# Kernel tuning notes

Hardware: AMD Instinct MI355X
Metric: run time of the kernel (lower is better)

Reference implementation:

```python
import jax, jax.numpy as jnp
import numpy as np

NUM_CODEBOOKS = 4
CODEBOOK_SIZE = 4096
CODEBOOK_DIM = 512


def setup_inputs() -> dict:
    key = jax.random.key(0)
    k1, k2 = jax.random.split(key)
    inputs = jax.random.normal(k1, (8, 2048, CODEBOOK_DIM), dtype=jnp.float32)
    # nn.init.uniform_(codebook.weight, -1/codebook_size, 1/codebook_size)
    bound = 1.0 / CODEBOOK_SIZE
    codebook = jax.random.uniform(k2, (CODEBOOK_SIZE, CODEBOOK_DIM),
                                  dtype=jnp.float32, minval=-bound, maxval=bound)
    return {"inputs": inputs, "codebook": codebook}


def reference(inputs, codebook):
    original_shape = inputs.shape
    x = inputs.reshape(-1, CODEBOOK_DIM)  # [N, D]
    cb_sq = jnp.sum(codebook ** 2, axis=1)  # [K]

    def stage(residual, _):
        # distances: ||r||^2 - 2 r.W^T + ||w||^2  -> [N, K]
        distances = (jnp.sum(residual ** 2, axis=1, keepdims=True)
                     - 2.0 * residual @ codebook.T
                     + cb_sq[None, :])
        indices = jnp.argmin(distances, axis=-1)  # [N]
        # one-hot matmul in torch == gather; same math
        quantized = codebook[indices]  # [N, D]
        # straight-through estimator
        q_ste = residual + jax.lax.stop_gradient(quantized - residual)
        new_residual = residual - q_ste
        return new_residual, (q_ste, indices)

    _, (q_stages, idx_stages) = jax.lax.scan(stage, x, None, length=NUM_CODEBOOKS)
    quantized_out = jnp.sum(q_stages, axis=0).reshape(original_shape)
    # all_indices stacked along last dim: [B, T, num_codebooks]
    all_indices = jnp.moveaxis(idx_stages, 0, -1).reshape(*original_shape[:-1], NUM_CODEBOOKS)
    vq_loss = jnp.float32(0.0)  # eval mode: self.training is False
    return quantized_out, all_indices, vq_loss
```

## Files before the change

### kernel.cpp

```cpp
#include <hip/hip_runtime.h>
#include <math.h>


namespace {
constexpr int N_ROWS     = 16384;
constexpr int DIM        = 512;
constexpr int K_CODES    = 4096;
constexpr int NUM_STAGES = 4;

constexpr int KTILES = 32;
constexpr float EPS  = 1e-3f;
constexpr int CAP    = 2;

constexpr int CROWS  = 32;
constexpr int CGRIDY = 8;
constexpr int WSTRC  = 68;
constexpr int RSTR   = 68;

constexpr size_t Q_OFF    = 0;
constexpr size_t IDX_OFF  = (size_t)N_ROWS * DIM;
constexpr size_t LOSS_OFF = IDX_OFF + (size_t)N_ROWS * NUM_STAGES;

constexpr size_t RES_OFF  = 0;
constexpr size_t RH_OFF   = (size_t)N_ROWS * DIM * 4;
constexpr size_t WH_OFF   = RH_OFF + (size_t)N_ROWS * DIM * 2;
constexpr size_t CBSQ_OFF = WH_OFF + (size_t)K_CODES * DIM * 2;
constexpr size_t RSQ_OFF  = CBSQ_OFF + (size_t)K_CODES * 4;
constexpr size_t PART_OFF = RSQ_OFF + (size_t)N_ROWS * 4;
constexpr size_t GBUF_OFF = PART_OFF + (size_t)N_ROWS * KTILES * 4;
constexpr size_t BCNT_OFF = GBUF_OFF + (size_t)N_ROWS * KTILES * CAP * 8;
constexpr size_t BENT_OFF = BCNT_OFF + 128;
constexpr size_t BEST_OFF = BENT_OFF + (size_t)KTILES * N_ROWS * 4;

constexpr unsigned long long EMPTY_E = 0xFFFFFFFFFFFFFFFFull;
constexpr unsigned long long OVFL_E  = 0xFFFFFFFFFFFFFFFEull;
}

typedef short bf16x8 __attribute__((ext_vector_type(8)));
typedef float f32x4  __attribute__((ext_vector_type(4)));

typedef __attribute__((address_space(1))) const unsigned int glob_u32;
typedef __attribute__((address_space(3))) unsigned int lds_u32;

__device__ __forceinline__ unsigned short f2bf(float x) {
    unsigned int u = __float_as_uint(x);
    return (unsigned short)((u + 0x7fffu + ((u >> 16) & 1u)) >> 16);
}

__device__ __forceinline__ float f4c(const float4& v, int q) {
    return q == 0 ? v.x : q == 1 ? v.y : q == 2 ? v.z : v.w;
}

__device__ __forceinline__ float rowsq_tree(const float v8[8], int lane) {
#pragma clang fp contract(off)
    float P[4];
#pragma unroll
    for (int b = 0; b < 4; ++b) {
        float xa = v8[2 * b];
        float xb = v8[2 * b + 1];
        float sa = xa * xa;
        float sb = xb * xb;
        float R  = sa + sb;
        float t  = R + __shfl_down(R, 16, 64);
        float u  = t + __shfl_down(t, 32, 64);
        float a  = u + __shfl_down(u, 8, 64);
        float c  = a + __shfl_down(a, 4, 64);
        float d  = c + __shfl_down(c, 2, 64);
        P[b]     = d + __shfl_down(d, 1, 64);
    }
    float s01 = P[0] + P[1];
    float s23 = P[2] + P[3];
    return s01 + s23;
}

__global__ __launch_bounds__(64)
void cbsq_wh_kernel(const float* __restrict__ cb, float* __restrict__ cb_sq,
                    unsigned short* __restrict__ wh, float* __restrict__ loss) {
    int k = blockIdx.x;
    int lane = threadIdx.x;
    const float* row = cb + (size_t)k * DIM;
    unsigned short* whp = wh + (size_t)k * DIM;
    float v8[8];
#pragma unroll
    for (int i = 0; i < 8; ++i) {
        float v = row[lane + i * 64];
        v8[i] = v;
        whp[lane + i * 64] = f2bf(v);
    }
    float s = rowsq_tree(v8, lane);
    if (lane == 0) cb_sq[k] = s;
    if (k == 0 && lane == 0) *loss = 0.0f;
}

__global__ __launch_bounds__(256)
void init_kernel(const float* __restrict__ input,
                 unsigned short* __restrict__ rh,
                 float* __restrict__ rsq, int* __restrict__ bcnt) {
    const int t = threadIdx.x;
    if (blockIdx.x == 0 && t < KTILES) bcnt[t] = 0;
    const int lane = t & 63;
    const int sub  = t >> 6;
    const int row  = blockIdx.x * 4 + sub;
    const float* x = input + (size_t)row * DIM;
    unsigned short* rhp = rh + (size_t)row * DIM;
    float v8[8];
#pragma unroll
    for (int i = 0; i < 8; ++i) {
        int d = lane + i * 64;
        float v = x[d];
        v8[i] = v;
        rhp[d] = f2bf(v);
    }
    float s = rowsq_tree(v8, lane);
    if (lane == 0) rsq[row] = s;
}

__global__ __launch_bounds__(256, 2)
void passA_kernel(const unsigned short* __restrict__ rh,
                  const unsigned short* __restrict__ wh,
                  const float* __restrict__ cb_sq,
                  const float* __restrict__ rsq,
                  float* __restrict__ part,
                  unsigned long long* __restrict__ gbuf) {
    const int lin = blockIdx.x + KTILES * blockIdx.y;
    const int xcd = lin & 7;
    const int c   = lin >> 3;
    const int jb  = c & 31;
    const int mb  = xcd * 16 + (c >> 5);
    const int mbase = mb * 128;
    const int nbase = jb * 128;

    __shared__ __align__(16) unsigned short At[128 * 64];
    __shared__ __align__(16) unsigned short Bt[128 * 64];
    __shared__ float rowmin[128][2];

    const int t    = threadIdx.x;
    const int lane = t & 63;
    const int wid  = t >> 6;
    const int wr   = wid >> 1;
    const int wc   = wid & 1;

    const int lrow = lane >> 3;
    const int d8g  = (lane & 7) ^ lrow;

    f32x4 acc[4][4];
#pragma unroll
    for (int mi = 0; mi < 4; ++mi)
#pragma unroll
        for (int ni = 0; ni < 4; ++ni) acc[mi][ni] = (f32x4){0.f, 0.f, 0.f, 0.f};

    for (int k0 = 0; k0 < DIM; k0 += 64) {
#pragma unroll
        for (int i = 0; i < 4; ++i) {
            int rbase = wid * 32 + i * 8;
            int grow  = rbase + lrow;
            const unsigned short* ga =
                rh + (size_t)(mbase + grow) * DIM + k0 + d8g * 8;
            __builtin_amdgcn_global_load_lds(
                (glob_u32*)ga, (lds_u32*)&At[rbase * 64], 16, 0, 0);
            const unsigned short* gb =
                wh + (size_t)(nbase + grow) * DIM + k0 + d8g * 8;
            __builtin_amdgcn_global_load_lds(
                (glob_u32*)gb, (lds_u32*)&Bt[rbase * 64], 16, 0, 0);
        }
        __syncthreads();

#pragma unroll
        for (int kk = 0; kk < 2; ++kk) {
            bf16x8 af[4], bfr[4];
            const int g = kk * 4 + (lane >> 4);
#pragma unroll
            for (int mi = 0; mi < 4; ++mi) {
                int row = wr * 64 + mi * 16 + (lane & 15);
                af[mi] = *(const bf16x8*)&At[row * 64 + (g ^ (row & 7)) * 8];
            }
#pragma unroll
            for (int ni = 0; ni < 4; ++ni) {
                int row = wc * 64 + ni * 16 + (lane & 15);
                bfr[ni] = *(const bf16x8*)&Bt[row * 64 + (g ^ (row & 7)) * 8];
            }
#pragma unroll
            for (int mi = 0; mi < 4; ++mi)
#pragma unroll
                for (int ni = 0; ni < 4; ++ni)
                    acc[mi][ni] = __builtin_amdgcn_mfma_f32_16x16x32_bf16(
                        af[mi], bfr[ni], acc[mi][ni], 0, 0, 0);
        }
        __syncthreads();
    }

    int* scnt = (int*)Bt;
    unsigned long long* sbuf = (unsigned long long*)At;
    if (t < 128) {
        scnt[t] = 0;
        sbuf[t * CAP + 0] = EMPTY_E;
        sbuf[t * CAP + 1] = EMPTY_E;
    }

#pragma unroll
    for (int mi = 0; mi < 4; ++mi) {
#pragma unroll
        for (int reg = 0; reg < 4; ++reg) {
            int rloc = wr * 64 + mi * 16 + (lane >> 4) * 4 + reg;
            float rsqv = rsq[mbase + rloc];
            float m = INFINITY;
#pragma unroll
            for (int ni = 0; ni < 4; ++ni) {
                int kg = nbase + wc * 64 + ni * 16 + (lane & 15);
                float y;
                {
#pragma clang fp contract(off)
                    float t2 = 2.0f * acc[mi][ni][reg];
                    float u  = rsqv - t2;
                    y        = u + cb_sq[kg];
                }
                m = fminf(m, y);
            }
#pragma unroll
            for (int off = 1; off < 16; off <<= 1)
                m = fminf(m, __shfl_xor(m, off, 64));
            if ((lane & 15) == 0) rowmin[rloc][wc] = m;
        }
    }
    __syncthreads();

#pragma unroll
    for (int mi = 0; mi < 4; ++mi) {
#pragma unroll
        for (int reg = 0; reg < 4; ++reg) {
            int rloc = wr * 64 + mi * 16 + (lane >> 4) * 4 + reg;
            float thrT = fminf(rowmin[rloc][0], rowmin[rloc][1]) + EPS;
            float rsqv = rsq[mbase + rloc];
#pragma unroll
            for (int ni = 0; ni < 4; ++ni) {
                int kg = nbase + wc * 64 + ni * 16 + (lane & 15);
                float y;
                {
#pragma clang fp contract(off)
                    float t2 = 2.0f * acc[mi][ni][reg];
                    float u  = rsqv - t2;
                    y        = u + cb_sq[kg];
                }
                if (y <= thrT) {
                    int pos = atomicAdd(&scnt[rloc], 1);
                    if (pos < CAP)
                        sbuf[rloc * CAP + pos] =
                            ((unsigned long long)__float_as_uint(y) << 32) |
                            (unsigned)kg;
                }
            }
        }
    }
    __syncthreads();

    if (t < 128) {
        part[(size_t)jb * N_ROWS + (mbase + t)] =
            fminf(rowmin[t][0], rowmin[t][1]);
        unsigned long long s0 = sbuf[t * CAP + 0];
        unsigned long long s1 = sbuf[t * CAP + 1];
        if (scnt[t] > CAP) s0 = OVFL_E;
        size_t bidx = ((size_t)jb * N_ROWS + (mbase + t)) * CAP;
        gbuf[bidx]     = s0;
        gbuf[bidx + 1] = s1;
    }
}

__global__ __launch_bounds__(256)
void passBC_kernel(const float* __restrict__ res,
                   const float* __restrict__ cb,
                   const float* __restrict__ cb_sq,
                   const float* __restrict__ rsq,
                   const float* __restrict__ part,
                   const unsigned long long* __restrict__ gbuf,
                   int* __restrict__ bcnt, int* __restrict__ bent,
                   unsigned long long* __restrict__ best) {
    const int t   = threadIdx.x;
    const int jr  = t & 31;
    const int rs  = t >> 5;
    const int row = blockIdx.x * 8 + rs;

    float pv = part[(size_t)jr * N_ROWS + row];
    float m = pv;
#pragma unroll
    for (int off = 1; off < 32; off <<= 1)
        m = fminf(m, __shfl_xor(m, off, 32));
    const float thr = m + EPS;

    unsigned long long s0 = EMPTY_E, s1 = EMPTY_E;
    bool surv = (pv <= thr);
    if (surv) {
        size_t bidx = ((size_t)jr * N_ROWS + row) * CAP;
        s0 = gbuf[bidx];
        s1 = gbuf[bidx + 1];
    }
    const bool ovfl = surv && (s0 == OVFL_E);
    if (ovfl) {
        int pos = atomicAdd(&bcnt[jr], 1);
        bent[(size_t)jr * N_ROWS + pos] = row;
    }

    int lcl = 0;
    unsigned long long cand = EMPTY_E;
    float y0 = __uint_as_float((unsigned)(s0 >> 32));
    float y1 = __uint_as_float((unsigned)(s1 >> 32));
    if (surv && !ovfl) {
        if (y0 <= thr) { lcl++; cand = s0; }
        if (y1 <= thr) { lcl++; cand = s1; }
    }
    int tot = lcl;
    int oc  = ovfl ? 1 : 0;
#pragma unroll
    for (int off = 1; off < 32; off <<= 1) {
        tot += __shfl_xor(tot, off, 32);
        oc  += __shfl_xor(oc, off, 32);
    }

    if (tot == 1 && oc == 0) {
        if (lcl == 1) best[row] = cand;
        return;
    }

    float by = INFINITY; int bk = 0x7fffffff;
    if (surv && !ovfl && lcl > 0) {
        const float* rr  = res + (size_t)row * DIM;
        const float rsqv = rsq[row];
#pragma unroll
        for (int sl = 0; sl < CAP; ++sl) {
            unsigned long long s = sl ? s1 : s0;
            float yh = __uint_as_float((unsigned)(s >> 32));
            if (!(yh <= thr)) continue;
            int k = (int)(s & 0xFFFFFFFFull);
            const float* wp = cb + (size_t)k * DIM;
            float dot = 0.0f;
#pragma unroll 8
            for (int d = 0; d < DIM; d += 4) {
                float4 r4 = *(const float4*)(rr + d);
                float4 w4 = *(const float4*)(wp + d);
                dot = fmaf(r4.x, w4.x, dot);
                dot = fmaf(r4.y, w4.y, dot);
                dot = fmaf(r4.z, w4.z, dot);
                dot = fmaf(r4.w, w4.w, dot);
            }
            float y;
            {
#pragma clang fp contract(off)
                float t2 = 2.0f * dot;
                float u  = rsqv - t2;
                y        = u + cb_sq[k];
            }
            if (y < by || (y == by && k < bk)) { by = y; bk = k; }
        }
    }

    unsigned long long pk =
        ((unsigned long long)__float_as_uint(by) << 32) | (unsigned)bk;
#pragma unroll
    for (int off = 1; off < 32; off <<= 1) {
        unsigned long long o =
            (unsigned long long)__shfl_xor((long long)pk, off, 32);
        if (o < pk) pk = o;
    }
    if (jr == 0) best[row] = pk;
}

__global__ __launch_bounds__(256)
void passC_kernel(const float* __restrict__ res,
                  const float* __restrict__ cb,
                  const float* __restrict__ cb_sq,
                  const float* __restrict__ rsq,
                  const int* __restrict__ bcnt, const int* __restrict__ bent,
                  unsigned long long* __restrict__ best) {
    const int j   = blockIdx.x;
    const int cnt = bcnt[j];
    const int t   = threadIdx.x;
    const int cg  = t & 31;
    const int rg  = t >> 5;

    __shared__ __align__(16) float Ws[128 * WSTRC];
    __shared__ __align__(16) float Rs[CROWS * RSTR];
    __shared__ int   rowl[CROWS];
    __shared__ float rsql[CROWS];

    for (int base = blockIdx.y * CROWS; base < cnt; base += gridDim.y * CROWS) {
        if (t < CROWS) {
            int e  = base + t;
            int rw = bent[(size_t)j * N_ROWS + (e < cnt ? e : cnt - 1)];
            rowl[t] = rw;
            rsql[t] = rsq[rw];
        }
        __syncthreads();
        const int nrows = min(CROWS, cnt - base);

        float acc[4][4];
#pragma unroll
        for (int ri = 0; ri < 4; ++ri)
#pragma unroll
            for (int q = 0; q < 4; ++q) acc[ri][q] = 0.0f;

        for (int d0 = 0; d0 < DIM; d0 += 64) {
#pragma unroll
            for (int p = 0; p < 8; ++p) {
                int idx  = p * 256 + t;
                int cand = idx >> 4;
                int d4   = idx & 15;
                float4 v = *(const float4*)(cb + (size_t)(j * 128 + cand) * DIM + d0 + d4 * 4);
                int s = d4 ^ ((cand >> 2) & 7) ^ ((cand >> 5) & 3);
                *(float4*)&Ws[cand * WSTRC + s * 4] = v;
            }
#pragma unroll
            for (int p = 0; p < 2; ++p) {
                int idx = p * 256 + t;
                int row = idx >> 4;
                int d4  = idx & 15;
                float4 v = *(const float4*)(res + (size_t)rowl[row] * DIM + d0 + d4 * 4);
                *(float4*)&Rs[row * RSTR + d4 * 4] = v;
            }
            __syncthreads();

#pragma unroll
            for (int dq = 0; dq < 16; ++dq) {
                const int s = dq ^ (cg & 7) ^ ((cg >> 3) & 3);
                float4 w4[4];
#pragma unroll
                for (int q = 0; q < 4; ++q)
                    w4[q] = *(const float4*)&Ws[(cg * 4 + q) * WSTRC + s * 4];
#pragma unroll
                for (int ri = 0; ri < 4; ++ri) {
                    float4 rf = *(const float4*)&Rs[(rg * 4 + ri) * RSTR + dq * 4];
#pragma unroll
                    for (int dd = 0; dd < 4; ++dd) {
                        float rv = f4c(rf, dd);
                        acc[ri][0] = fmaf(rv, f4c(w4[0], dd), acc[ri][0]);
                        acc[ri][1] = fmaf(rv, f4c(w4[1], dd), acc[ri][1]);
                        acc[ri][2] = fmaf(rv, f4c(w4[2], dd), acc[ri][2]);
                        acc[ri][3] = fmaf(rv, f4c(w4[3], dd), acc[ri][3]);
                    }
                }
            }
            __syncthreads();
        }

#pragma unroll
        for (int ri = 0; ri < 4; ++ri) {
            int rloc = rg * 4 + ri;
            float rsqv = rsql[rloc];
            float by = INFINITY; int bk = 0x7fffffff;
#pragma unroll
            for (int q = 0; q < 4; ++q) {
                int k = j * 128 + cg * 4 + q;
                float y;
                {
#pragma clang fp contract(off)
                    float t2 = 2.0f * acc[ri][q];
                    float u  = rsqv - t2;
                    y        = u + cb_sq[k];
                }
                if (y < by || (y == by && k < bk)) { by = y; bk = k; }
            }
#pragma unroll
            for (int off = 1; off < 32; off <<= 1) {
                float ov = __shfl_xor(by, off, 64);
                int   oi = __shfl_xor(bk, off, 64);
                if (ov < by || (ov == by && oi < bk)) { by = ov; bk = oi; }
            }
            if (cg == 0 && rloc < nrows) {
                unsigned long long pk =
                    ((unsigned long long)__float_as_uint(by) << 32) |
                    (unsigned long long)(unsigned)bk;
                atomicMin(&best[rowl[rloc]], pk);
            }
        }
        __syncthreads();
    }
}

__global__ __launch_bounds__(256)
void combine_kernel(float* __restrict__ res_out,
                    const float* __restrict__ res_in,
                    const float* __restrict__ cb,
                    const unsigned long long* __restrict__ best,
                    float* __restrict__ qout,
                    float* __restrict__ idx_out,
                    unsigned short* __restrict__ rh,
                    float* __restrict__ rsq,
                    int* __restrict__ bcnt,
                    int stage, int do_next) {
#pragma clang fp contract(off)
    const int t    = threadIdx.x;
    if (do_next && blockIdx.x == 0 && t < KTILES) bcnt[t] = 0;
    const int lane = t & 63;
    const int sub  = t >> 6;
    const int row  = blockIdx.x * 4 + sub;

    int bi = (int)(best[row] & 0xffffffffull);
    if (lane == 0) idx_out[(size_t)row * NUM_STAGES + stage] = (float)bi;

    const float* w   = cb + (size_t)bi * DIM;
    const float* rin = res_in + (size_t)row * DIM;
    float*       r   = res_out + (size_t)row * DIM;
    float*       q   = qout + (size_t)row * DIM;
    unsigned short* rhp = rh + (size_t)row * DIM;

    float rn8[8];
#pragma unroll
    for (int i = 0; i < DIM / 64; ++i) {
        int d = lane + i * 64;
        float wv = w[d];
        float rv = rin[d];
        float tq    = wv - rv;
        float q_ste = rv + tq;
        float rn    = rv - q_ste;
        rn8[i] = rn;
        if (do_next) {
            r[d]   = rn;
            rhp[d] = f2bf(rn);
        }
        if (stage == 0) q[d] = q_ste;
        else            q[d] = q[d] + q_ste;
    }
    if (do_next) {
        float s = rowsq_tree(rn8, lane);
        if (lane == 0) rsq[row] = s;
    }
}

extern "C" void kernel_launch(void* const* d_in, const int* in_sizes, int n_in,
                              void* d_out, int out_size, void* d_ws, size_t ws_size,
                              hipStream_t stream) {
    const float* input = (const float*)d_in[0];
    const float* cb    = (const float*)d_in[1];

    float* out_f   = (float*)d_out;
    float* qout    = out_f + Q_OFF;
    float* idx_out = out_f + IDX_OFF;
    float* loss    = out_f + LOSS_OFF;

    char* ws = (char*)d_ws;
    float*          residual = (float*)(ws + RES_OFF);
    unsigned short* rh       = (unsigned short*)(ws + RH_OFF);
    unsigned short* wh       = (unsigned short*)(ws + WH_OFF);
    float*          cb_sq    = (float*)(ws + CBSQ_OFF);
    float*          rsq      = (float*)(ws + RSQ_OFF);
    float*          part     = (float*)(ws + PART_OFF);
    unsigned long long* gbuf = (unsigned long long*)(ws + GBUF_OFF);
    int*            bcnt     = (int*)(ws + BCNT_OFF);
    int*            bent     = (int*)(ws + BENT_OFF);
    unsigned long long* best = (unsigned long long*)(ws + BEST_OFF);

    cbsq_wh_kernel<<<K_CODES, 64, 0, stream>>>(cb, cb_sq, wh, loss);
    init_kernel<<<N_ROWS / 4, 256, 0, stream>>>(input, rh, rsq, bcnt);

    for (int s = 0; s < NUM_STAGES; ++s) {
        const float* rin = (s == 0) ? input : residual;
        passA_kernel<<<dim3(KTILES, N_ROWS / 128), 256, 0, stream>>>(
            rh, wh, cb_sq, rsq, part, gbuf);
        passBC_kernel<<<N_ROWS / 8, 256, 0, stream>>>(
            rin, cb, cb_sq, rsq, part, gbuf, bcnt, bent, best);
        passC_kernel<<<dim3(KTILES, CGRIDY), 256, 0, stream>>>(
            rin, cb, cb_sq, rsq, bcnt, bent, best);
        combine_kernel<<<N_ROWS / 4, 256, 0, stream>>>(
            residual, rin, cb, best, qout, idx_out, rh, rsq, bcnt,
            s, (s < NUM_STAGES - 1) ? 1 : 0);
    }
}
```

Measured before the change: 916.3 us.

## Fuse candidate resolution, overflow rescan and residual update into one kernel

Replaces the per-stage passBC, passC and combine kernels with a single finish kernel. A 32-lane group per row resolves the argmin. When a tile's candidate buffer overflowed, that group rescans the tile's 128 codes inline with fp32 dot products. It then immediately writes the index, quantized output, residual, bf16 residual and row norm. This removes two launches per stage, the best/bcnt/bent round-trips and atomics, at the cost of serial per-row fp32 work when overflows occur instead of the tiled LDS passC.

```diff
diff --git a/kernel.cpp b/kernel.cpp
--- a/kernel.cpp
+++ b/kernel.cpp
@@ -11,11 +11,6 @@
 constexpr int KTILES = 32;
 constexpr float EPS  = 1e-3f;
 constexpr int CAP    = 2;
-
-constexpr int CROWS  = 32;
-constexpr int CGRIDY = 8;
-constexpr int WSTRC  = 68;
-constexpr int RSTR   = 68;
 
 constexpr size_t Q_OFF    = 0;
 constexpr size_t IDX_OFF  = (size_t)N_ROWS * DIM;
@@ -28,9 +23,6 @@
 constexpr size_t RSQ_OFF  = CBSQ_OFF + (size_t)K_CODES * 4;
 constexpr size_t PART_OFF = RSQ_OFF + (size_t)N_ROWS * 4;
 constexpr size_t GBUF_OFF = PART_OFF + (size_t)N_ROWS * KTILES * 4;
-constexpr size_t BCNT_OFF = GBUF_OFF + (size_t)N_ROWS * KTILES * CAP * 8;
-constexpr size_t BENT_OFF = BCNT_OFF + 128;
-constexpr size_t BEST_OFF = BENT_OFF + (size_t)KTILES * N_ROWS * 4;
 
 constexpr unsigned long long EMPTY_E = 0xFFFFFFFFFFFFFFFFull;
 constexpr unsigned long long OVFL_E  = 0xFFFFFFFFFFFFFFFEull;
@@ -45,10 +37,6 @@
 __device__ __forceinline__ unsigned short f2bf(float x) {
     unsigned int u = __float_as_uint(x);
     return (unsigned short)((u + 0x7fffu + ((u >> 16) & 1u)) >> 16);
-}
-
-__device__ __forceinline__ float f4c(const float4& v, int q) {
-    return q == 0 ? v.x : q == 1 ? v.y : q == 2 ? v.z : v.w;
 }
 
 __device__ __forceinline__ float rowsq_tree(const float v8[8], int lane) {
@@ -95,9 +83,8 @@
 __global__ __launch_bounds__(256)
 void init_kernel(const float* __restrict__ input,
                  unsigned short* __restrict__ rh,
-                 float* __restrict__ rsq, int* __restrict__ bcnt) {
+                 float* __restrict__ rsq) {
     const int t = threadIdx.x;
-    if (blockIdx.x == 0 && t < KTILES) bcnt[t] = 0;
     const int lane = t & 63;
     const int sub  = t >> 6;
     const int row  = blockIdx.x * 4 + sub;
@@ -266,14 +253,18 @@
 }
 
 __global__ __launch_bounds__(256)
-void passBC_kernel(const float* __restrict__ res,
+void finish_kernel(float* __restrict__ res,
+                   const float* __restrict__ rin,
                    const float* __restrict__ cb,
                    const float* __restrict__ cb_sq,
-                   const float* __restrict__ rsq,
+                   float* __restrict__ rsq,
                    const float* __restrict__ part,
                    const unsigned long long* __restrict__ gbuf,
-                   int* __restrict__ bcnt, int* __restrict__ bent,
-                   unsigned long long* __restrict__ best) {
+                   float* __restrict__ qout,
+                   float* __restrict__ idx_out,
+                   unsigned short* __restrict__ rh,
+                   int stage, int do_next) {
+#pragma clang fp contract(off)
     const int t   = threadIdx.x;
     const int jr  = t & 31;
     const int rs  = t >> 5;
@@ -294,10 +285,6 @@
         s1 = gbuf[bidx + 1];
     }
     const bool ovfl = surv && (s0 == OVFL_E);
-    if (ovfl) {
-        int pos = atomicAdd(&bcnt[jr], 1);
-        bent[(size_t)jr * N_ROWS + pos] = row;
-    }
 
     int lcl = 0;
     unsigned long long cand = EMPTY_E;
@@ -315,212 +302,122 @@
         oc  += __shfl_xor(oc, off, 32);
     }
 
+    const float* rr  = rin + (size_t)row * DIM;
+    const float rsqv = rsq[row];
+
+    unsigned long long lpk;
     if (tot == 1 && oc == 0) {
-        if (lcl == 1) best[row] = cand;
-        return;
-    }
-
-    float by = INFINITY; int bk = 0x7fffffff;
-    if (surv && !ovfl && lcl > 0) {
-        const float* rr  = res + (size_t)row * DIM;
-        const float rsqv = rsq[row];
-#pragma unroll
-        for (int sl = 0; sl < CAP; ++sl) {
-            unsigned long long s = sl ? s1 : s0;
-            float yh = __uint_as_float((unsigned)(s >> 32));
-            if (!(yh <= thr)) continue;
-            int k = (int)(s & 0xFFFFFFFFull);
-            const float* wp = cb + (size_t)k * DIM;
-            float dot = 0.0f;
+        lpk = (lcl == 1) ? cand : EMPTY_E;
+    } else {
+        float by = INFINITY; int bk = 0x7fffffff;
+        if (surv && !ovfl && lcl > 0) {
+#pragma unroll
+            for (int sl = 0; sl < CAP; ++sl) {
+                unsigned long long s = sl ? s1 : s0;
+                float yh = __uint_as_float((unsigned)(s >> 32));
+                if (!(yh <= thr)) continue;
+                int k = (int)(s & 0xFFFFFFFFull);
+                const float* wp = cb + (size_t)k * DIM;
+                float dot = 0.0f;
 #pragma unroll 8
-            for (int d = 0; d < DIM; d += 4) {
-                float4 r4 = *(const float4*)(rr + d);
-                float4 w4 = *(const float4*)(wp + d);
-                dot = fmaf(r4.x, w4.x, dot);
-                dot = fmaf(r4.y, w4.y, dot);
-                dot = fmaf(r4.z, w4.z, dot);
-                dot = fmaf(r4.w, w4.w, dot);
-            }
-            float y;
-            {
-#pragma clang fp contract(off)
+                for (int d = 0; d < DIM; d += 4) {
+                    float4 r4 = *(const float4*)(rr + d);
+                    float4 w4 = *(const float4*)(wp + d);
+                    dot = fmaf(r4.x, w4.x, dot);
+                    dot = fmaf(r4.y, w4.y, dot);
+                    dot = fmaf(r4.z, w4.z, dot);
+                    dot = fmaf(r4.w, w4.w, dot);
+                }
                 float t2 = 2.0f * dot;
                 float u  = rsqv - t2;
-                y        = u + cb_sq[k];
-            }
-            if (y < by || (y == by && k < bk)) { by = y; bk = k; }
-        }
-    }
-
-    unsigned long long pk =
-        ((unsigned long long)__float_as_uint(by) << 32) | (unsigned)bk;
+                float y  = u + cb_sq[k];
+                if (y < by || (y == by && k < bk)) { by = y; bk = k; }
+            }
+        }
+        unsigned grp = (unsigned)(__ballot(ovfl) >> (t & 32));
+        while (grp) {
+            int jt = __builtin_ctz(grp);
+            grp &= grp - 1;
+#pragma unroll
+            for (int q = 0; q < 4; ++q) {
+                int k = jt * 128 + jr * 4 + q;
+                const float* wp = cb + (size_t)k * DIM;
+                float dot = 0.0f;
+#pragma unroll 8
+                for (int d = 0; d < DIM; d += 4) {
+                    float4 r4 = *(const float4*)(rr + d);
+                    float4 w4 = *(const float4*)(wp + d);
+                    dot = fmaf(r4.x, w4.x, dot);
+                    dot = fmaf(r4.y, w4.y, dot);
+                    dot = fmaf(r4.z, w4.z, dot);
+                    dot = fmaf(r4.w, w4.w, dot);
+                }
+                float t2 = 2.0f * dot;
+                float u  = rsqv - t2;
+                float y  = u + cb_sq[k];
+                if (y < by || (y == by && k < bk)) { by = y; bk = k; }
+            }
+        }
+        lpk = ((unsigned long long)__float_as_uint(by) << 32) | (unsigned)bk;
+    }
+
 #pragma unroll
     for (int off = 1; off < 32; off <<= 1) {
         unsigned long long o =
-            (unsigned long long)__shfl_xor((long long)pk, off, 32);
-        if (o < pk) pk = o;
-    }
-    if (jr == 0) best[row] = pk;
-}
-
-__global__ __launch_bounds__(256)
-void passC_kernel(const float* __restrict__ res,
-                  const float* __restrict__ cb,
-                  const float* __restrict__ cb_sq,
-                  const float* __restrict__ rsq,
-                  const int* __restrict__ bcnt, const int* __restrict__ bent,
-                  unsigned long long* __restrict__ best) {
-    const int j   = blockIdx.x;
-    const int cnt = bcnt[j];
-    const int t   = threadIdx.x;
-    const int cg  = t & 31;
-    const int rg  = t >> 5;
-
-    __shared__ __align__(16) float Ws[128 * WSTRC];
-    __shared__ __align__(16) float Rs[CROWS * RSTR];
-    __shared__ int   rowl[CROWS];
-    __shared__ float rsql[CROWS];
-
-    for (int base = blockIdx.y * CROWS; base < cnt; base += gridDim.y * CROWS) {
-        if (t < CROWS) {
-            int e  = base + t;
-            int rw = bent[(size_t)j * N_ROWS + (e < cnt ? e : cnt - 1)];
-            rowl[t] = rw;
-            rsql[t] = rsq[rw];
-        }
-        __syncthreads();
-        const int nrows = min(CROWS, cnt - base);
-
-        float acc[4][4];
-#pragma unroll
-        for (int ri = 0; ri < 4; ++ri)
-#pragma unroll
-            for (int q = 0; q < 4; ++q) acc[ri][q] = 0.0f;
-
-        for (int d0 = 0; d0 < DIM; d0 += 64) {
-#pragma unroll
-            for (int p = 0; p < 8; ++p) {
-                int idx  = p * 256 + t;
-                int cand = idx >> 4;
-                int d4   = idx & 15;
-                float4 v = *(const float4*)(cb + (size_t)(j * 128 + cand) * DIM + d0 + d4 * 4);
-                int s = d4 ^ ((cand >> 2) & 7) ^ ((cand >> 5) & 3);
-                *(float4*)&Ws[cand * WSTRC + s * 4] = v;
-            }
-#pragma unroll
-            for (int p = 0; p < 2; ++p) {
-                int idx = p * 256 + t;
-                int row = idx >> 4;
-                int d4  = idx & 15;
-                float4 v = *(const float4*)(res + (size_t)rowl[row] * DIM + d0 + d4 * 4);
-                *(float4*)&Rs[row * RSTR + d4 * 4] = v;
-            }
-            __syncthreads();
-
-#pragma unroll
-            for (int dq = 0; dq < 16; ++dq) {
-                const int s = dq ^ (cg & 7) ^ ((cg >> 3) & 3);
-                float4 w4[4];
-#pragma unroll
-                for (int q = 0; q < 4; ++q)
-                    w4[q] = *(const float4*)&Ws[(cg * 4 + q) * WSTRC + s * 4];
-#pragma unroll
-                for (int ri = 0; ri < 4; ++ri) {
-                    float4 rf = *(const float4*)&Rs[(rg * 4 + ri) * RSTR + dq * 4];
-#pragma unroll
-                    for (int dd = 0; dd < 4; ++dd) {
-                        float rv = f4c(rf, dd);
-                        acc[ri][0] = fmaf(rv, f4c(w4[0], dd), acc[ri][0]);
-                        acc[ri][1] = fmaf(rv, f4c(w4[1], dd), acc[ri][1]);
-                        acc[ri][2] = fmaf(rv, f4c(w4[2], dd), acc[ri][2]);
-                        acc[ri][3] = fmaf(rv, f4c(w4[3], dd), acc[ri][3]);
-                    }
-                }
-            }
-            __syncthreads();
-        }
-
-#pragma unroll
-        for (int ri = 0; ri < 4; ++ri) {
-            int rloc = rg * 4 + ri;
-            float rsqv = rsql[rloc];
-            float by = INFINITY; int bk = 0x7fffffff;
-#pragma unroll
-            for (int q = 0; q < 4; ++q) {
-                int k = j * 128 + cg * 4 + q;
-                float y;
-                {
-#pragma clang fp contract(off)
-                    float t2 = 2.0f * acc[ri][q];
-                    float u  = rsqv - t2;
-                    y        = u + cb_sq[k];
-                }
-                if (y < by || (y == by && k < bk)) { by = y; bk = k; }
-            }
-#pragma unroll
-            for (int off = 1; off < 32; off <<= 1) {
-                float ov = __shfl_xor(by, off, 64);
-                int   oi = __shfl_xor(bk, off, 64);
-                if (ov < by || (ov == by && oi < bk)) { by = ov; bk = oi; }
-            }
-            if (cg == 0 && rloc < nrows) {
-                unsigned long long pk =
-                    ((unsigned long long)__float_as_uint(by) << 32) |
-                    (unsigned long long)(unsigned)bk;
-                atomicMin(&best[rowl[rloc]], pk);
-            }
-        }
-        __syncthreads();
-    }
-}
-
-__global__ __launch_bounds__(256)
-void combine_kernel(float* __restrict__ res_out,
-                    const float* __restrict__ res_in,
-                    const float* __restrict__ cb,
-                    const unsigned long long* __restrict__ best,
-                    float* __restrict__ qout,
-                    float* __restrict__ idx_out,
-                    unsigned short* __restrict__ rh,
-                    float* __restrict__ rsq,
-                    int* __restrict__ bcnt,
-                    int stage, int do_next) {
-#pragma clang fp contract(off)
-    const int t    = threadIdx.x;
-    if (do_next && blockIdx.x == 0 && t < KTILES) bcnt[t] = 0;
-    const int lane = t & 63;
-    const int sub  = t >> 6;
-    const int row  = blockIdx.x * 4 + sub;
-
-    int bi = (int)(best[row] & 0xffffffffull);
-    if (lane == 0) idx_out[(size_t)row * NUM_STAGES + stage] = (float)bi;
-
-    const float* w   = cb + (size_t)bi * DIM;
-    const float* rin = res_in + (size_t)row * DIM;
-    float*       r   = res_out + (size_t)row * DIM;
-    float*       q   = qout + (size_t)row * DIM;
+            (unsigned long long)__shfl_xor((long long)lpk, off, 32);
+        if (o < lpk) lpk = o;
+    }
+    const int bi = (int)(lpk & 0xFFFFFFFFull);
+    if (jr == 0) idx_out[(size_t)row * NUM_STAGES + stage] = (float)bi;
+
+    const float* wp = cb + (size_t)bi * DIM;
+    float*       rp = res + (size_t)row * DIM;
+    float*       qp = qout + (size_t)row * DIM;
     unsigned short* rhp = rh + (size_t)row * DIM;
 
-    float rn8[8];
-#pragma unroll
-    for (int i = 0; i < DIM / 64; ++i) {
-        int d = lane + i * 64;
-        float wv = w[d];
-        float rv = rin[d];
+    float rn16[16];
+#pragma unroll
+    for (int i = 0; i < 16; ++i) {
+        int d = jr + 32 * i;
+        float wv = wp[d];
+        float rv = rr[d];
         float tq    = wv - rv;
         float q_ste = rv + tq;
         float rn    = rv - q_ste;
-        rn8[i] = rn;
+        rn16[i] = rn;
         if (do_next) {
-            r[d]   = rn;
+            rp[d]  = rn;
             rhp[d] = f2bf(rn);
         }
-        if (stage == 0) q[d] = q_ste;
-        else            q[d] = q[d] + q_ste;
-    }
+        if (stage == 0) qp[d] = q_ste;
+        else            qp[d] = qp[d] + q_ste;
+    }
+
     if (do_next) {
-        float s = rowsq_tree(rn8, lane);
-        if (lane == 0) rsq[row] = s;
+        float P[4];
+#pragma unroll
+        for (int b = 0; b < 4; ++b) {
+            float xa_lo = rn16[4 * b + 0];
+            float xb_lo = rn16[4 * b + 2];
+            float xa_hi = rn16[4 * b + 1];
+            float xb_hi = rn16[4 * b + 3];
+            float sa_lo = xa_lo * xa_lo;
+            float sb_lo = xb_lo * xb_lo;
+            float R_lo  = sa_lo + sb_lo;
+            float sa_hi = xa_hi * xa_hi;
+            float sb_hi = xb_hi * xb_hi;
+            float R_hi  = sa_hi + sb_hi;
+            float t_lo = R_lo + __shfl_down(R_lo, 16, 32);
+            float t_hi = R_hi + __shfl_down(R_hi, 16, 32);
+            float u  = t_lo + t_hi;
+            float a  = u + __shfl_down(u, 8, 32);
+            float cc = a + __shfl_down(a, 4, 32);
+            float dd = cc + __shfl_down(cc, 2, 32);
+            P[b]     = dd + __shfl_down(dd, 1, 32);
+        }
+        float s01 = P[0] + P[1];
+        float s23 = P[2] + P[3];
+        if (jr == 0) rsq[row] = s01 + s23;
     }
 }
 
@@ -543,23 +440,16 @@
     float*          rsq      = (float*)(ws + RSQ_OFF);
     float*          part     = (float*)(ws + PART_OFF);
     unsigned long long* gbuf = (unsigned long long*)(ws + GBUF_OFF);
-    int*            bcnt     = (int*)(ws + BCNT_OFF);
-    int*            bent     = (int*)(ws + BENT_OFF);
-    unsigned long long* best = (unsigned long long*)(ws + BEST_OFF);
 
     cbsq_wh_kernel<<<K_CODES, 64, 0, stream>>>(cb, cb_sq, wh, loss);
-    init_kernel<<<N_ROWS / 4, 256, 0, stream>>>(input, rh, rsq, bcnt);
+    init_kernel<<<N_ROWS / 4, 256, 0, stream>>>(input, rh, rsq);
 
     for (int s = 0; s < NUM_STAGES; ++s) {
         const float* rin = (s == 0) ? input : residual;
         passA_kernel<<<dim3(KTILES, N_ROWS / 128), 256, 0, stream>>>(
             rh, wh, cb_sq, rsq, part, gbuf);
-        passBC_kernel<<<N_ROWS / 8, 256, 0, stream>>>(
-            rin, cb, cb_sq, rsq, part, gbuf, bcnt, bent, best);
-        passC_kernel<<<dim3(KTILES, CGRIDY), 256, 0, stream>>>(
-            rin, cb, cb_sq, rsq, bcnt, bent, best);
-        combine_kernel<<<N_ROWS / 4, 256, 0, stream>>>(
-            residual, rin, cb, best, qout, idx_out, rh, rsq, bcnt,
-            s, (s < NUM_STAGES - 1) ? 1 : 0);
-    }
-}
+        finish_kernel<<<N_ROWS / 8, 256, 0, stream>>>(
+            residual, rin, cb, cb_sq, rsq, part, gbuf,
+            qout, idx_out, rh, s, (s < NUM_STAGES - 1) ? 1 : 0);
+    }
+}
```

Result: faster. 864.4 us (-5.7%).
